# Kernel tuning notes

Hardware: AMD Instinct MI355X
Metric: run time of the kernel (lower is better)

Reference implementation:

```python
import jax, jax.numpy as jnp
import numpy as np

B, S, F, H = 256, 512, 64, 128
ODE_STEPS = 4
MAX_DT = 1.0


def setup_inputs() -> dict:
    key = jax.random.key(0)
    ks = jax.random.split(key, 11)
    D = F + H  # concat(x_t, h) width
    xav = float(np.sqrt(6.0 / (D + H)))          # xavier_uniform for gate weights
    bsc = float(1.0 / np.sqrt(D))                # torch Linear default bias init
    x = jax.random.normal(ks[0], (B, S, F), jnp.float32)
    time_diffs = jax.random.uniform(ks[1], (B, S), jnp.float32, 0.1, 2.0)
    def w(k):
        return jax.random.uniform(k, (D, H), jnp.float32, -xav, xav)
    def b(k):
        return jax.random.uniform(k, (H,), jnp.float32, -bsc, bsc)
    return {
        "x": x, "time_diffs": time_diffs,
        "W_i": w(ks[2]), "b_i": b(ks[3]),
        "W_f": w(ks[4]), "b_f": b(ks[5]),
        "W_o": w(ks[6]), "b_o": b(ks[7]),
        "W_g": w(ks[8]), "b_g": b(ks[9]),
    }


def reference(x, time_diffs, W_i, b_i, W_f, b_f, W_o, b_o, W_g, b_g):
    def ode_func(x_t, h, c):
        comb = jnp.concatenate([x_t, h], axis=-1)  # [B, F+H]
        i = jax.nn.sigmoid(comb @ W_i + b_i)
        f = jax.nn.sigmoid(comb @ W_f + b_f)
        o = jax.nn.sigmoid(comb @ W_o + b_o)
        g = jnp.tanh(comb @ W_g + b_g)
        dc = i * g + f * c - c
        dh = o * jnp.tanh(c) - h
        return dh, dc

    def rk4_step(x_t, h, c, dt):  # dt: [B, 1]
        k1h, k1c = ode_func(x_t, h, c)
        k2h, k2c = ode_func(x_t, h + 0.5 * dt * k1h, c + 0.5 * dt * k1c)
        k3h, k3c = ode_func(x_t, h + 0.5 * dt * k2h, c + 0.5 * dt * k2c)
        k4h, k4c = ode_func(x_t, h + dt * k3h, c + dt * k3c)
        h_new = h + dt / 6.0 * (k1h + 2 * k2h + 2 * k3h + k4h)
        c_new = c + dt / 6.0 * (k1c + 2 * k2c + 2 * k3c + k4c)
        return h_new, c_new

    def time_step(carry, inp):
        h, c = carry
        x_t, dtv = inp  # x_t [B,F], dtv [B]
        sub_dt = (jnp.minimum(dtv, MAX_DT) / ODE_STEPS)[:, None]  # [B,1]
        def body(hc, _):
            hh, cc = hc
            return rk4_step(x_t, hh, cc, sub_dt), None
        (h, c), _ = jax.lax.scan(body, (h, c), None, length=ODE_STEPS)
        return (h, c), h

    h0 = jnp.zeros((x.shape[0], H), x.dtype)
    c0 = jnp.zeros((x.shape[0], H), x.dtype)
    xs = (jnp.swapaxes(x, 0, 1), jnp.swapaxes(time_diffs, 0, 1))  # [S,B,F], [S,B]
    _, hs = jax.lax.scan(time_step, (h0, c0), xs)  # [S,B,H]
    return jnp.swapaxes(hs, 0, 1)  # [B,S,H]
```

## Files before the change

### kernel.cpp

```cpp
#include <hip/hip_runtime.h>


#define B_N 256
#define S_N 512
#define F_N 64
#define H_N 128

typedef _Float16 v8h __attribute__((ext_vector_type(8)));
typedef float v4f __attribute__((ext_vector_type(4)));

#define PIN_V(x) asm("" : "+v"(x))

static __device__ __forceinline__ float sigm(float x) {
  float e = __builtin_amdgcn_exp2f(-1.442695040888963f * x);
  return __builtin_amdgcn_rcpf(1.0f + e);
}

__global__ void __launch_bounds__(512, 2) clstm_mfma4(
    const float* __restrict__ x,
    const float* __restrict__ td,
    const float* __restrict__ Wi, const float* __restrict__ bi,
    const float* __restrict__ Wf, const float* __restrict__ bff,
    const float* __restrict__ Wo, const float* __restrict__ bo,
    const float* __restrict__ Wg, const float* __restrict__ bg,
    float* __restrict__ out)
{
  const int b    = blockIdx.x;
  const int t    = threadIdx.x;
  const int wv   = t >> 6;
  const int l    = t & 63;
  const int col  = l & 15;
  const int quad = l >> 4;
  const int n    = wv * 16 + col;

  const float* Wptr[4] = {Wi, Wf, Wo, Wg};

  v8h Bh[4][4];
  v8h Bx[4][2];
#pragma unroll
  for (int g = 0; g < 4; ++g) {
    const float* W = Wptr[g];
#pragma unroll
    for (int kt = 0; kt < 4; ++kt) {
      v8h f;
#pragma unroll
      for (int j = 0; j < 8; ++j)
        f[j] = (_Float16)W[(64 + kt * 32 + quad * 8 + j) * H_N + n];
      Bh[g][kt] = f;
      PIN_V(Bh[g][kt]);
    }
#pragma unroll
    for (int kt = 0; kt < 2; ++kt) {
      v8h f;
#pragma unroll
      for (int j = 0; j < 8; ++j)
        f[j] = (_Float16)W[(kt * 32 + quad * 8 + j) * H_N + n];
      Bx[g][kt] = f;
      PIN_V(Bx[g][kt]);
    }
  }
  float bias[4];
#pragma unroll
  for (int g = 0; g < 4; ++g)
    bias[g] = (g == 0 ? bi : g == 1 ? bff : g == 2 ? bo : bg)[n];

  __shared__ alignas(16) _Float16 lds_h[2][H_N];
  __shared__ alignas(16) _Float16 lds_x[F_N];
  __shared__ float lds_td[S_N];

  lds_td[t] = td[b * S_N + t];
  if (t < 32) {
    const float* xr = x + (size_t)b * S_N * F_N;
    lds_x[2 * t]     = (_Float16)xr[2 * t];
    lds_x[2 * t + 1] = (_Float16)xr[2 * t + 1];
  }
  if (t < H_N) lds_h[0][t] = (_Float16)0.0f;
  __syncthreads();

  float h0v = 0.f, c0v = 0.f;
  float h_ev = 0.f, c_ev = 0.f;
  float sum_h = 0.f, sum_c = 0.f;
  const v4f zf = {0.f, 0.f, 0.f, 0.f};

  for (int s = 0; s < S_N; ++s) {
    float dt  = fminf(lds_td[s], 1.0f) * 0.25f;
    float hdt = 0.5f * dt;
    float d6  = dt * (1.0f / 6.0f);

    v8h ax0 = *(const v8h*)(lds_x + quad * 8);
    v8h ax1 = *(const v8h*)(lds_x + 32 + quad * 8);
    v4f xpD[4];
#pragma unroll
    for (int g = 0; g < 4; ++g) {
      float bv = bias[g];
      v4f cbv = {bv, bv, bv, bv};
      v4f a = __builtin_amdgcn_mfma_f32_16x16x32_f16(ax0, Bx[g][0], cbv, 0, 0, 0);
      xpD[g] = __builtin_amdgcn_mfma_f32_16x16x32_f16(ax1, Bx[g][1], a, 0, 0, 0);
    }

    float xn0 = 0.f, xn1 = 0.f;
    if (t < 32 && s + 1 < S_N) {
      const float* xr = x + (size_t)(b * S_N + s + 1) * F_N;
      xn0 = xr[2 * t]; xn1 = xr[2 * t + 1];
    }

#pragma unroll
    for (int ode = 0; ode < 4; ++ode) {
#pragma unroll
      for (int st = 0; st < 4; ++st) {
        const _Float16* hb = lds_h[st & 1];
        v8h ah0 = *(const v8h*)(hb + quad * 8);
        v8h ah1 = *(const v8h*)(hb + 32 + quad * 8);
        v8h ah2 = *(const v8h*)(hb + 64 + quad * 8);
        v8h ah3 = *(const v8h*)(hb + 96 + quad * 8);

        float pre[4];
#pragma unroll
        for (int g = 0; g < 4; ++g) {
          v4f c02 = __builtin_amdgcn_mfma_f32_16x16x32_f16(ah0, Bh[g][0], xpD[g], 0, 0, 0);
          c02 = __builtin_amdgcn_mfma_f32_16x16x32_f16(ah1, Bh[g][1], c02, 0, 0, 0);
          v4f c13 = __builtin_amdgcn_mfma_f32_16x16x32_f16(ah2, Bh[g][2], zf, 0, 0, 0);
          c13 = __builtin_amdgcn_mfma_f32_16x16x32_f16(ah3, Bh[g][3], c13, 0, 0, 0);
          pre[g] = c02[0] + c13[0];
        }

        float ai = sigm(pre[0]);
        float af = sigm(pre[1]);
        float ao = sigm(pre[2]);
        float ag = fmaf(2.0f, sigm(2.0f * pre[3]), -1.0f);
        float tc = fmaf(2.0f, sigm(2.0f * c_ev), -1.0f);
        float kc = fmaf(ai, ag, (af - 1.0f) * c_ev);
        float kh = fmaf(ao, tc, -h_ev);

        float hnx, cnx;
        if (st == 0 || st == 1) {
          hnx = fmaf(hdt, kh, h0v); cnx = fmaf(hdt, kc, c0v);
        } else if (st == 2) {
          hnx = fmaf(dt, kh, h0v); cnx = fmaf(dt, kc, c0v);
        } else {
          float sh = sum_h + kh, sc = sum_c + kc;
          h0v = fmaf(d6, sh, h0v); c0v = fmaf(d6, sc, c0v);
          hnx = h0v; cnx = c0v;
        }

        if (quad == 0) lds_h[(st & 1) ^ 1][n] = (_Float16)hnx;
        if (st == 3 && ode == 3 && t < 32 && s + 1 < S_N) {
          lds_x[2 * t]     = (_Float16)xn0;
          lds_x[2 * t + 1] = (_Float16)xn1;
        }
        __syncthreads();

        if (st == 0) {
          sum_h = kh; sum_c = kc;
        } else if (st == 1 || st == 2) {
          sum_h = fmaf(2.f, kh, sum_h); sum_c = fmaf(2.f, kc, sum_c);
        }
        h_ev = hnx; c_ev = cnx;
      }
    }

    if (quad == 0) out[(size_t)(b * S_N + s) * H_N + n] = h0v;
  }
}

extern "C" void kernel_launch(void* const* d_in, const int* in_sizes, int n_in,
                              void* d_out, int out_size, void* d_ws, size_t ws_size,
                              hipStream_t stream) {
  (void)in_sizes; (void)n_in; (void)d_ws; (void)ws_size; (void)out_size;
  clstm_mfma4<<<B_N, 512, 0, stream>>>(
      (const float*)d_in[0],
      (const float*)d_in[1],
      (const float*)d_in[2], (const float*)d_in[3],
      (const float*)d_in[4], (const float*)d_in[5],
      (const float*)d_in[6], (const float*)d_in[7],
      (const float*)d_in[8], (const float*)d_in[9],
      (float*)d_out);
}
```

Before: 3.674 ms.

## Software-pipeline the c-state update behind the o-gate MFMAs in the RK4 recurrence

```diff
diff --git a/kernel.cpp b/kernel.cpp
--- a/kernel.cpp
+++ b/kernel.cpp
@@ -10,13 +10,14 @@
 typedef float v4f __attribute__((ext_vector_type(4)));
 
 #define PIN_V(x) asm("" : "+v"(x))
+#define MFMA16(a, b, c) __builtin_amdgcn_mfma_f32_16x16x32_f16((a), (b), (c), 0, 0, 0)
 
 static __device__ __forceinline__ float sigm(float x) {
   float e = __builtin_amdgcn_exp2f(-1.442695040888963f * x);
   return __builtin_amdgcn_rcpf(1.0f + e);
 }
 
-__global__ void __launch_bounds__(512, 2) clstm_mfma4(
+__global__ void __launch_bounds__(512, 2) clstm_mfma5(
     const float* __restrict__ x,
     const float* __restrict__ td,
     const float* __restrict__ Wi, const float* __restrict__ bi,
@@ -75,91 +76,116 @@
     lds_x[2 * t + 1] = (_Float16)xr[2 * t + 1];
   }
   if (t < H_N) lds_h[0][t] = (_Float16)0.0f;
-  __syncthreads();
 
   float h0v = 0.f, c0v = 0.f;
   float h_ev = 0.f, c_ev = 0.f;
   float sum_h = 0.f, sum_c = 0.f;
+  float tc = 0.f;
+  float dt = 0.f, hdt = 0.f, d6 = 0.f, d6p = 0.f;
   const v4f zf = {0.f, 0.f, 0.f, 0.f};
+  v4f ci2 = zf, ci3 = zf, cf2 = zf, cf3 = zf, cg2 = zf, cg3 = zf;
+  v4f xpD[4] = {zf, zf, zf, zf};
+  float xn0 = 0.f, xn1 = 0.f;
 
   for (int s = 0; s < S_N; ++s) {
-    float dt  = fminf(lds_td[s], 1.0f) * 0.25f;
-    float hdt = 0.5f * dt;
-    float d6  = dt * (1.0f / 6.0f);
-
-    v8h ax0 = *(const v8h*)(lds_x + quad * 8);
-    v8h ax1 = *(const v8h*)(lds_x + 32 + quad * 8);
-    v4f xpD[4];
-#pragma unroll
-    for (int g = 0; g < 4; ++g) {
-      float bv = bias[g];
-      v4f cbv = {bv, bv, bv, bv};
-      v4f a = __builtin_amdgcn_mfma_f32_16x16x32_f16(ax0, Bx[g][0], cbv, 0, 0, 0);
-      xpD[g] = __builtin_amdgcn_mfma_f32_16x16x32_f16(ax1, Bx[g][1], a, 0, 0, 0);
-    }
-
-    float xn0 = 0.f, xn1 = 0.f;
-    if (t < 32 && s + 1 < S_N) {
-      const float* xr = x + (size_t)(b * S_N + s + 1) * F_N;
-      xn0 = xr[2 * t]; xn1 = xr[2 * t + 1];
-    }
-
 #pragma unroll
     for (int ode = 0; ode < 4; ++ode) {
 #pragma unroll
       for (int st = 0; st < 4; ++st) {
+        __syncthreads();
         const _Float16* hb = lds_h[st & 1];
         v8h ah0 = *(const v8h*)(hb + quad * 8);
         v8h ah1 = *(const v8h*)(hb + 32 + quad * 8);
         v8h ah2 = *(const v8h*)(hb + 64 + quad * 8);
         v8h ah3 = *(const v8h*)(hb + 96 + quad * 8);
 
-        float pre[4];
-#pragma unroll
-        for (int g = 0; g < 4; ++g) {
-          v4f c02 = __builtin_amdgcn_mfma_f32_16x16x32_f16(ah0, Bh[g][0], xpD[g], 0, 0, 0);
-          c02 = __builtin_amdgcn_mfma_f32_16x16x32_f16(ah1, Bh[g][1], c02, 0, 0, 0);
-          v4f c13 = __builtin_amdgcn_mfma_f32_16x16x32_f16(ah2, Bh[g][2], zf, 0, 0, 0);
-          c13 = __builtin_amdgcn_mfma_f32_16x16x32_f16(ah3, Bh[g][3], c13, 0, 0, 0);
-          pre[g] = c02[0] + c13[0];
-        }
-
-        float ai = sigm(pre[0]);
-        float af = sigm(pre[1]);
-        float ao = sigm(pre[2]);
-        float ag = fmaf(2.0f, sigm(2.0f * pre[3]), -1.0f);
-        float tc = fmaf(2.0f, sigm(2.0f * c_ev), -1.0f);
-        float kc = fmaf(ai, ag, (af - 1.0f) * c_ev);
+        if (ode == 0 && st == 0) {
+          dt  = fminf(lds_td[s], 1.0f) * 0.25f;
+          hdt = 0.5f * dt;
+          d6  = dt * (1.0f / 6.0f);
+          v8h ax0 = *(const v8h*)(lds_x + quad * 8);
+          v8h ax1 = *(const v8h*)(lds_x + 32 + quad * 8);
+#pragma unroll
+          for (int g = 0; g < 4; ++g) {
+            float bv = bias[g];
+            v4f cbv = {bv, bv, bv, bv};
+            v4f a = MFMA16(ax0, Bx[g][0], cbv);
+            xpD[g] = MFMA16(ax1, Bx[g][1], a);
+          }
+          xn0 = 0.f; xn1 = 0.f;
+          if (t < 32 && s + 1 < S_N) {
+            const float* xr = x + (size_t)(b * S_N + s + 1) * F_N;
+            xn0 = xr[2 * t]; xn1 = xr[2 * t + 1];
+          }
+        }
+
+        {
+          const int pr = (st == 0) ? 3 : st - 1;
+          float pi = ci2[0] + ci3[0];
+          float pf = cf2[0] + cf3[0];
+          float pg = cg2[0] + cg3[0];
+          float ai = sigm(pi);
+          float af = sigm(pf);
+          float ag = fmaf(2.0f, sigm(2.0f * pg), -1.0f);
+          float kc = fmaf(ai, ag, (af - 1.0f) * c_ev);
+          float cnx;
+          if (pr == 0)      { sum_c = kc;                      cnx = fmaf(hdt, kc, c0v); }
+          else if (pr == 1) { sum_c = fmaf(2.f, kc, sum_c);    cnx = fmaf(hdt, kc, c0v); }
+          else if (pr == 2) { sum_c = fmaf(2.f, kc, sum_c);    cnx = fmaf(dt, kc, c0v); }
+          else {
+            float sc = sum_c + kc;
+            float dd = (ode == 0 && st == 0) ? d6p : d6;
+            c0v = fmaf(dd, sc, c0v);
+            cnx = c0v;
+          }
+          c_ev = cnx;
+          tc = fmaf(2.0f, sigm(2.0f * c_ev), -1.0f);
+        }
+
+        v4f co2 = MFMA16(ah0, Bh[2][0], xpD[2]);
+        co2     = MFMA16(ah1, Bh[2][1], co2);
+        v4f co3 = MFMA16(ah2, Bh[2][2], zf);
+        co3     = MFMA16(ah3, Bh[2][3], co3);
+        __builtin_amdgcn_sched_barrier(0);
+
+        ci2 = MFMA16(ah0, Bh[0][0], xpD[0]);
+        ci2 = MFMA16(ah1, Bh[0][1], ci2);
+        ci3 = MFMA16(ah2, Bh[0][2], zf);
+        ci3 = MFMA16(ah3, Bh[0][3], ci3);
+        cf2 = MFMA16(ah0, Bh[1][0], xpD[1]);
+        cf2 = MFMA16(ah1, Bh[1][1], cf2);
+        cf3 = MFMA16(ah2, Bh[1][2], zf);
+        cf3 = MFMA16(ah3, Bh[1][3], cf3);
+        cg2 = MFMA16(ah0, Bh[3][0], xpD[3]);
+        cg2 = MFMA16(ah1, Bh[3][1], cg2);
+        cg3 = MFMA16(ah2, Bh[3][2], zf);
+        cg3 = MFMA16(ah3, Bh[3][3], cg3);
+
+        float po = co2[0] + co3[0];
+        float ao = sigm(po);
         float kh = fmaf(ao, tc, -h_ev);
-
-        float hnx, cnx;
-        if (st == 0 || st == 1) {
-          hnx = fmaf(hdt, kh, h0v); cnx = fmaf(hdt, kc, c0v);
-        } else if (st == 2) {
-          hnx = fmaf(dt, kh, h0v); cnx = fmaf(dt, kc, c0v);
-        } else {
-          float sh = sum_h + kh, sc = sum_c + kc;
-          h0v = fmaf(d6, sh, h0v); c0v = fmaf(d6, sc, c0v);
-          hnx = h0v; cnx = c0v;
-        }
-
+        float hnx;
+        if (st == 0)      { sum_h = kh;                      hnx = fmaf(hdt, kh, h0v); }
+        else if (st == 1) { sum_h = fmaf(2.f, kh, sum_h);    hnx = fmaf(hdt, kh, h0v); }
+        else if (st == 2) { sum_h = fmaf(2.f, kh, sum_h);    hnx = fmaf(dt, kh, h0v); }
+        else {
+          float sh = sum_h + kh;
+          h0v = fmaf(d6, sh, h0v);
+          hnx = h0v;
+        }
+        h_ev = hnx;
         if (quad == 0) lds_h[(st & 1) ^ 1][n] = (_Float16)hnx;
-        if (st == 3 && ode == 3 && t < 32 && s + 1 < S_N) {
-          lds_x[2 * t]     = (_Float16)xn0;
-          lds_x[2 * t + 1] = (_Float16)xn1;
-        }
-        __syncthreads();
-
-        if (st == 0) {
-          sum_h = kh; sum_c = kc;
-        } else if (st == 1 || st == 2) {
-          sum_h = fmaf(2.f, kh, sum_h); sum_c = fmaf(2.f, kc, sum_c);
-        }
-        h_ev = hnx; c_ev = cnx;
+
+        if (ode == 3 && st == 3) {
+          if (t < 32 && s + 1 < S_N) {
+            lds_x[2 * t]     = (_Float16)xn0;
+            lds_x[2 * t + 1] = (_Float16)xn1;
+          }
+          if (quad == 0) out[(size_t)(b * S_N + s) * H_N + n] = h0v;
+          d6p = d6;
+        }
       }
     }
-
-    if (quad == 0) out[(size_t)(b * S_N + s) * H_N + n] = h0v;
   }
 }
 
@@ -167,7 +193,7 @@
                               void* d_out, int out_size, void* d_ws, size_t ws_size,
                               hipStream_t stream) {
   (void)in_sizes; (void)n_in; (void)d_ws; (void)ws_size; (void)out_size;
-  clstm_mfma4<<<B_N, 512, 0, stream>>>(
+  clstm_mfma5<<<B_N, 512, 0, stream>>>(
       (const float*)d_in[0],
       (const float*)d_in[1],
       (const float*)d_in[2], (const float*)d_in[3],
```

Result: faster. 3.447 ms (-6.2%).
